# Performance work log

Hardware: AMD Instinct MI355X
Metric: run time of the kernel (lower is better)

The kernel has to match this reference:

```python
import jax, jax.numpy as jnp
import numpy as np

# Dimensions
BATCH = 4
NUM_NODE = 20000
NUM_EDGE = 1280000   # avg degree 64
K = 2                # num_rd_kernels
NUM_SEQ = 13         # num_sequence (13 time points -> 12 intervals)
SEQ_IN = 12
RES = 2              # fixed-step Euler substeps per interval (resolution)
TEMP = 1.0           # temperature for gate softmax
NUM_OUT = -12        # num_output_sequence slice


def setup_inputs() -> dict:
    key = jax.random.key(0)
    ks = jax.random.split(key, 6)
    inputs = jax.random.normal(ks[0], (BATCH, 1, NUM_NODE, SEQ_IN), dtype=jnp.float32)
    gate = jax.random.normal(ks[1], (NUM_SEQ - 1, K), dtype=jnp.float32)
    # edge list from adjacency CSV (from/to columns)
    src = jax.random.randint(ks[2], (NUM_EDGE,), 0, NUM_NODE)
    dst = jax.random.randint(ks[3], (NUM_EDGE,), 0, NUM_NODE)
    # learned per-kernel parameters of multi_reaction_diffusion
    w = jax.random.normal(ks[4], (K, NUM_EDGE), dtype=jnp.float32) * 0.1  # edge diffusivity logits
    r = jax.random.normal(ks[5], (K, NUM_NODE), dtype=jnp.float32) * 0.1  # node reaction coeffs
    return {"inputs": inputs, "gate": gate, "w": w, "r": r, "src": src, "dst": dst}


def _dxdt(x, g, w, r, src, dst):
    # x: [B,N]  g: [K]  w: [K,E]  r: [K,N]
    a = jax.nn.sigmoid(w)                                   # [K,E] edge diffusivity
    xs = x[:, src]                                          # [B,E]
    xd = x[:, dst]                                          # [B,E]
    msg = a[:, None, :] * (xs - xd)[None, :, :]             # [K,B,E]
    # scatter-add messages into destination nodes
    diff = jax.ops.segment_sum(jnp.moveaxis(msg, 2, 0), dst, num_segments=NUM_NODE)  # [N,K,B]
    diff = jnp.transpose(diff, (1, 2, 0))                   # [K,B,N]
    react = r[:, None, :] * x[None] * (1.0 - x[None])       # [K,B,N] logistic reaction
    return jnp.einsum('k,kbn->bn', g, diff + react)         # gate-weighted mix of RD kernels


def reference(inputs, gate, w, r, src, dst):
    x0 = inputs[:, 0, :, -1]                                # [B,N]
    dt = 1.0 / (NUM_SEQ - 1)
    h = jnp.float32(dt / RES)
    gates = jax.nn.softmax(gate / TEMP, axis=-1)            # [NUM_SEQ-1, K]

    def interval(x, g):
        def step(xc, _):
            return xc + h * _dxdt(xc, g, w, r, src, dst), None
        x, _ = jax.lax.scan(step, x, None, length=RES)
        return x, x

    _, traj = jax.lax.scan(interval, x0, gates)             # [NUM_SEQ-1, B, N]
    out = jnp.concatenate([x0[None], traj], axis=0)         # [NUM_SEQ, B, N]
    return out[NUM_OUT:]                                    # last 12 horizons
```

## Files before the change

kernel.cpp:

```cpp
#include <hip/hip_runtime.h>
#include <hip/hip_fp16.h>
#include <math.h>

#define NNODE 20000
#define NEDGE 1280000
#define HSTEP (1.0f/24.0f)
#define NBUCK 313
#define CAP   4608
#define EPB   2048

__global__ void rd_init(const float* __restrict__ inp,
                        float4* __restrict__ x,
                        int* __restrict__ cursor) {
    int n = blockIdx.x * blockDim.x + threadIdx.x;
    if (n < NBUCK) cursor[n] = n * CAP;
    if (n < NNODE) {
        float4 v;
        v.x = inp[0 * NNODE * 12 + n * 12 + 11];
        v.y = inp[1 * NNODE * 12 + n * 12 + 11];
        v.z = inp[2 * NNODE * 12 + n * 12 + 11];
        v.w = inp[3 * NNODE * 12 + n * 12 + 11];
        x[n] = v;
    }
}

__global__ __launch_bounds__(256) void rd_part(const int* __restrict__ src,
                                               const int* __restrict__ dst,
                                               const float* __restrict__ w,
                                               int* __restrict__ cursor,
                                               uint2* __restrict__ rec) {
    __shared__ int h[4][NBUCK];
    int wv = threadIdx.x >> 6;
    for (int i = threadIdx.x; i < 4 * NBUCK; i += 256) ((int*)h)[i] = 0;
    __syncthreads();
    int e0 = blockIdx.x * EPB;
    #pragma unroll
    for (int k = 0; k < 8; ++k) {
        int e = e0 + k * 256 + threadIdx.x;
        if (e < NEDGE) atomicAdd(&h[wv][dst[e] >> 6], 1);
    }
    __syncthreads();
    for (int i = threadIdx.x; i < NBUCK; i += 256) {
        int c0 = h[0][i], c1 = h[1][i], c2 = h[2][i], c3 = h[3][i];
        int tot = c0 + c1 + c2 + c3;
        int gb = tot ? atomicAdd(&cursor[i], tot) : 0;
        h[0][i] = gb;
        h[1][i] = gb + c0;
        h[2][i] = gb + c0 + c1;
        h[3][i] = gb + c0 + c1 + c2;
    }
    __syncthreads();
    #pragma unroll
    for (int k = 0; k < 8; ++k) {
        int e = e0 + k * 256 + threadIdx.x;
        if (e < NEDGE) {
            int d = dst[e];
            int b = d >> 6;
            int p = atomicAdd(&h[wv][b], 1);
            float s0 = 1.0f / (1.0f + expf(-w[e]));
            float s1 = 1.0f / (1.0f + expf(-w[NEDGE + e]));
            __half2 hh = __floats2half2_rn(s0, s1);
            uint2 q;
            q.x = (unsigned)src[e] | ((unsigned)(d & 63) << 16);
            q.y = *(unsigned*)&hh;
            if (p < (b + 1) * CAP) rec[p] = q;
        }
    }
}

__global__ void rd_bscan(const int* __restrict__ cursor, int* __restrict__ boff) {
    int lane = threadIdx.x;
    int carry = 0;
    #pragma unroll
    for (int c = 0; c < 5; ++c) {
        int i = c * 64 + lane;
        int v = (i < NBUCK) ? (cursor[i] - i * CAP) : 0;
        int incl = v;
        #pragma unroll
        for (int o = 1; o < 64; o <<= 1) {
            int u = __shfl_up(incl, o, 64);
            if (lane >= o) incl += u;
        }
        if (i < NBUCK) boff[i] = carry + incl - v;
        carry += __shfl(incl, 63, 64);
    }
    if (lane == 0) boff[NBUCK] = carry;
}

__global__ __launch_bounds__(256) void rd_bsort(const uint2* __restrict__ rec,
                                                const int* __restrict__ cursor,
                                                const int* __restrict__ boff,
                                                unsigned short* __restrict__ es16,
                                                unsigned* __restrict__ ew32,
                                                int* __restrict__ offsets) {
    __shared__ uint2 rs[CAP];
    __shared__ int h[64], excl[64];
    int b = blockIdx.x;
    int ib = b * CAP;
    int cnt = cursor[b] - ib; if (cnt > CAP) cnt = CAP;
    int ob = boff[b];
    if (threadIdx.x < 64) h[threadIdx.x] = 0;
    __syncthreads();
    for (int i = threadIdx.x; i < cnt; i += 256) {
        uint2 q = rec[ib + i];
        rs[i] = q;
        atomicAdd(&h[(q.x >> 16) & 63], 1);
    }
    __syncthreads();
    if (threadIdx.x < 64) {
        int lane = threadIdx.x;
        int v = h[lane];
        int incl = v;
        #pragma unroll
        for (int o = 1; o < 64; o <<= 1) {
            int u = __shfl_up(incl, o, 64);
            if (lane >= o) incl += u;
        }
        excl[lane] = incl - v;
        int n = b * 64 + lane;
        if (n < NNODE) offsets[n] = ob + excl[lane];
        h[lane] = 0;
    }
    if (b == NBUCK - 1 && threadIdx.x == 0) offsets[NNODE] = NEDGE;
    __syncthreads();
    for (int i = threadIdx.x; i < cnt; i += 256) {
        uint2 q = rs[i];
        int dl = (q.x >> 16) & 63;
        int rank = atomicAdd(&h[dl], 1);
        int p = ob + excl[dl] + rank;
        es16[p] = (unsigned short)(q.x & 0xFFFFu);
        ew32[p] = q.y;
    }
}

__global__ __launch_bounds__(256) void rd_step(
        const float4* __restrict__ xin, float4* __restrict__ xout,
        const unsigned short* __restrict__ es16,
        const unsigned* __restrict__ ew32,
        const int* __restrict__ offsets,
        const float* __restrict__ r, const float* __restrict__ gate,
        int itv, int write_out, float* __restrict__ out) {
    int tid  = blockIdx.x * 256 + threadIdx.x;
    int node = tid >> 4;
    int sub  = threadIdx.x & 15;
    float ga = gate[2 * itv], gb = gate[2 * itv + 1];
    float g0 = 1.0f / (1.0f + expf(gb - ga));
    float g1 = 1.0f - g0;

    int beg = offsets[node], end = offsets[node + 1];
    float4 acc = make_float4(0.f, 0.f, 0.f, 0.f);
    float wsum = 0.f;

    int j = beg + sub;
    bool valid = j < end;
    unsigned s = 0, wb = 0;
    if (valid) { s = es16[j]; wb = ew32[j]; }
    while (valid) {
        float4 xs = xin[s];
        int jn = j + 16;
        bool vn = jn < end;
        unsigned s2 = 0, wb2 = 0;
        if (vn) { s2 = es16[jn]; wb2 = ew32[jn]; }
        __half2 hh = *(__half2*)&wb;
        float2 f = __half22float2(hh);
        float we = fmaf(g0, f.x, g1 * f.y);
        acc.x = fmaf(we, xs.x, acc.x);
        acc.y = fmaf(we, xs.y, acc.y);
        acc.z = fmaf(we, xs.z, acc.z);
        acc.w = fmaf(we, xs.w, acc.w);
        wsum += we;
        j = jn; s = s2; wb = wb2; valid = vn;
    }
    #pragma unroll
    for (int m = 8; m >= 1; m >>= 1) {
        acc.x += __shfl_xor(acc.x, m, 64);
        acc.y += __shfl_xor(acc.y, m, 64);
        acc.z += __shfl_xor(acc.z, m, 64);
        acc.w += __shfl_xor(acc.w, m, 64);
        wsum  += __shfl_xor(wsum,  m, 64);
    }
    float4 xd = xin[node];
    float rc = fmaf(g0, r[node], g1 * r[NNODE + node]);
    float4 xn;
    xn.x = xd.x + HSTEP * ((acc.x - wsum * xd.x) + rc * xd.x * (1.0f - xd.x));
    xn.y = xd.y + HSTEP * ((acc.y - wsum * xd.y) + rc * xd.y * (1.0f - xd.y));
    xn.z = xd.z + HSTEP * ((acc.z - wsum * xd.z) + rc * xd.z * (1.0f - xd.z));
    xn.w = xd.w + HSTEP * ((acc.w - wsum * xd.w) + rc * xd.w * (1.0f - xd.w));
    if (sub == 0) xout[node] = xn;
    if (write_out && sub < 4) {
        float v = (sub == 0) ? xn.x : (sub == 1) ? xn.y : (sub == 2) ? xn.z : xn.w;
        out[(itv * 4 + sub) * NNODE + node] = v;
    }
}

extern "C" void kernel_launch(void* const* d_in, const int* in_sizes, int n_in,
                              void* d_out, int out_size, void* d_ws, size_t ws_size,
                              hipStream_t stream) {
    const float* inp  = (const float*)d_in[0];
    const float* gate = (const float*)d_in[1];
    const float* w    = (const float*)d_in[2];
    const float* r    = (const float*)d_in[3];
    const int*   src  = (const int*)d_in[4];
    const int*   dst  = (const int*)d_in[5];
    float* out = (float*)d_out;

    char* ws = (char*)d_ws;
    float4*         xA      = (float4*)(ws + 0);
    float4*         xB      = (float4*)(ws + 320512);
    int*            offsets = (int*)   (ws + 641024);
    int*            cursor  = (int*)   (ws + 721152);
    int*            boff    = (int*)   (ws + 722432);
    uint2*          rec     = (uint2*) (ws + 723712);
    unsigned short* es16    = (unsigned short*)(ws + 12262144);
    unsigned*       ew32    = (unsigned*)(ws + 14822144);

    rd_init <<<(NNODE + 255) / 256, 256, 0, stream>>>(inp, xA, cursor);
    rd_part <<<(NEDGE + EPB - 1) / EPB, 256, 0, stream>>>(src, dst, w, cursor, rec);
    rd_bscan<<<1, 64, 0, stream>>>(cursor, boff);
    rd_bsort<<<NBUCK, 256, 0, stream>>>(rec, cursor, boff, es16, ew32, offsets);

    float4* xin = xA;
    float4* xout = xB;
    for (int itv = 0; itv < 12; ++itv) {
        for (int s = 0; s < 2; ++s) {
            rd_step<<<NNODE * 16 / 256, 256, 0, stream>>>(xin, xout, es16, ew32,
                                                          offsets, r, gate, itv, s, out);
            float4* t = xin; xin = xout; xout = t;
        }
    }
}
```

Baseline: 265.2 us.

## Vectorize edge partitioning, cache ranks in LDS, widen bsort, unroll gather loop

```diff
diff --git a/kernel.cpp b/kernel.cpp
--- a/kernel.cpp
+++ b/kernel.cpp
@@ -24,23 +24,32 @@
     }
 }
 
-__global__ __launch_bounds__(256) void rd_part(const int* __restrict__ src,
-                                               const int* __restrict__ dst,
-                                               const float* __restrict__ w,
+__global__ __launch_bounds__(256) void rd_part(const int4* __restrict__ src4,
+                                               const int4* __restrict__ dst4,
+                                               const float4* __restrict__ w4,
                                                int* __restrict__ cursor,
                                                uint2* __restrict__ rec) {
     __shared__ int h[4][NBUCK];
-    int wv = threadIdx.x >> 6;
-    for (int i = threadIdx.x; i < 4 * NBUCK; i += 256) ((int*)h)[i] = 0;
-    __syncthreads();
-    int e0 = blockIdx.x * EPB;
-    #pragma unroll
-    for (int k = 0; k < 8; ++k) {
-        int e = e0 + k * 256 + threadIdx.x;
-        if (e < NEDGE) atomicAdd(&h[wv][dst[e] >> 6], 1);
-    }
-    __syncthreads();
-    for (int i = threadIdx.x; i < NBUCK; i += 256) {
+    __shared__ uint4 cache[EPB / 4];
+    int t = threadIdx.x, wv = t >> 6;
+    for (int i = t; i < 4 * NBUCK; i += 256) ((int*)h)[i] = 0;
+    __syncthreads();
+    int q0 = blockIdx.x * (EPB / 4);
+    #pragma unroll
+    for (int k = 0; k < 2; ++k) {
+        int qi = q0 + k * 256 + t;
+        int4 d4 = dst4[qi];
+        int dd[4] = {d4.x, d4.y, d4.z, d4.w};
+        unsigned cc[4];
+        #pragma unroll
+        for (int u = 0; u < 4; ++u) {
+            int rank = atomicAdd(&h[wv][dd[u] >> 6], 1);
+            cc[u] = (unsigned)dd[u] | ((unsigned)rank << 15);
+        }
+        cache[k * 256 + t] = make_uint4(cc[0], cc[1], cc[2], cc[3]);
+    }
+    __syncthreads();
+    for (int i = t; i < NBUCK; i += 256) {
         int c0 = h[0][i], c1 = h[1][i], c2 = h[2][i], c3 = h[3][i];
         int tot = c0 + c1 + c2 + c3;
         int gb = tot ? atomicAdd(&cursor[i], tot) : 0;
@@ -51,19 +60,29 @@
     }
     __syncthreads();
     #pragma unroll
-    for (int k = 0; k < 8; ++k) {
-        int e = e0 + k * 256 + threadIdx.x;
-        if (e < NEDGE) {
-            int d = dst[e];
+    for (int k = 0; k < 2; ++k) {
+        int qi = q0 + k * 256 + t;
+        int4 s4 = src4[qi];
+        float4 wa = w4[qi];
+        float4 wb = w4[NEDGE / 4 + qi];
+        uint4 c4 = cache[k * 256 + t];
+        int ss[4] = {s4.x, s4.y, s4.z, s4.w};
+        float fa[4] = {wa.x, wa.y, wa.z, wa.w};
+        float fb[4] = {wb.x, wb.y, wb.z, wb.w};
+        unsigned cc[4] = {c4.x, c4.y, c4.z, c4.w};
+        #pragma unroll
+        for (int u = 0; u < 4; ++u) {
+            int d = cc[u] & 0x7FFF;
+            int rank = (int)(cc[u] >> 15);
             int b = d >> 6;
-            int p = atomicAdd(&h[wv][b], 1);
-            float s0 = 1.0f / (1.0f + expf(-w[e]));
-            float s1 = 1.0f / (1.0f + expf(-w[NEDGE + e]));
+            int p = h[wv][b] + rank;
+            float s0 = 1.0f / (1.0f + expf(-fa[u]));
+            float s1 = 1.0f / (1.0f + expf(-fb[u]));
             __half2 hh = __floats2half2_rn(s0, s1);
-            uint2 q;
-            q.x = (unsigned)src[e] | ((unsigned)(d & 63) << 16);
-            q.y = *(unsigned*)&hh;
-            if (p < (b + 1) * CAP) rec[p] = q;
+            uint2 rq;
+            rq.x = (unsigned)ss[u] | ((unsigned)(d & 63) << 16);
+            rq.y = *(unsigned*)&hh;
+            if (p < (b + 1) * CAP) rec[p] = rq;
         }
     }
 }
@@ -87,7 +106,7 @@
     if (lane == 0) boff[NBUCK] = carry;
 }
 
-__global__ __launch_bounds__(256) void rd_bsort(const uint2* __restrict__ rec,
+__global__ __launch_bounds__(512) void rd_bsort(const uint2* __restrict__ rec,
                                                 const int* __restrict__ cursor,
                                                 const int* __restrict__ boff,
                                                 unsigned short* __restrict__ es16,
@@ -101,7 +120,7 @@
     int ob = boff[b];
     if (threadIdx.x < 64) h[threadIdx.x] = 0;
     __syncthreads();
-    for (int i = threadIdx.x; i < cnt; i += 256) {
+    for (int i = threadIdx.x; i < cnt; i += 512) {
         uint2 q = rec[ib + i];
         rs[i] = q;
         atomicAdd(&h[(q.x >> 16) & 63], 1);
@@ -123,7 +142,7 @@
     }
     if (b == NBUCK - 1 && threadIdx.x == 0) offsets[NNODE] = NEDGE;
     __syncthreads();
-    for (int i = threadIdx.x; i < cnt; i += 256) {
+    for (int i = threadIdx.x; i < cnt; i += 512) {
         uint2 q = rs[i];
         int dl = (q.x >> 16) & 63;
         int rank = atomicAdd(&h[dl], 1);
@@ -148,28 +167,55 @@
     float g1 = 1.0f - g0;
 
     int beg = offsets[node], end = offsets[node + 1];
+    float4 xd = xin[node];
+    float rc = fmaf(g0, r[node], g1 * r[NNODE + node]);
+
     float4 acc = make_float4(0.f, 0.f, 0.f, 0.f);
     float wsum = 0.f;
-
     int j = beg + sub;
-    bool valid = j < end;
-    unsigned s = 0, wb = 0;
-    if (valid) { s = es16[j]; wb = ew32[j]; }
-    while (valid) {
-        float4 xs = xin[s];
-        int jn = j + 16;
-        bool vn = jn < end;
-        unsigned s2 = 0, wb2 = 0;
-        if (vn) { s2 = es16[jn]; wb2 = ew32[jn]; }
-        __half2 hh = *(__half2*)&wb;
-        float2 f = __half22float2(hh);
-        float we = fmaf(g0, f.x, g1 * f.y);
-        acc.x = fmaf(we, xs.x, acc.x);
-        acc.y = fmaf(we, xs.y, acc.y);
-        acc.z = fmaf(we, xs.z, acc.z);
-        acc.w = fmaf(we, xs.w, acc.w);
-        wsum += we;
-        j = jn; s = s2; wb = wb2; valid = vn;
+    for (; j + 48 < end; j += 64) {
+        unsigned a0 = es16[j], a1 = es16[j + 16], a2 = es16[j + 32], a3 = es16[j + 48];
+        unsigned b0 = ew32[j], b1 = ew32[j + 16], b2 = ew32[j + 32], b3 = ew32[j + 48];
+        float4 x0 = xin[a0], x1 = xin[a1], x2 = xin[a2], x3 = xin[a3];
+        float2 f0 = __half22float2(*(__half2*)&b0);
+        float2 f1 = __half22float2(*(__half2*)&b1);
+        float2 f2 = __half22float2(*(__half2*)&b2);
+        float2 f3 = __half22float2(*(__half2*)&b3);
+        float we0 = fmaf(g0, f0.x, g1 * f0.y);
+        float we1 = fmaf(g0, f1.x, g1 * f1.y);
+        float we2 = fmaf(g0, f2.x, g1 * f2.y);
+        float we3 = fmaf(g0, f3.x, g1 * f3.y);
+        acc.x = fmaf(we0, x0.x, fmaf(we1, x1.x, fmaf(we2, x2.x, fmaf(we3, x3.x, acc.x))));
+        acc.y = fmaf(we0, x0.y, fmaf(we1, x1.y, fmaf(we2, x2.y, fmaf(we3, x3.y, acc.y))));
+        acc.z = fmaf(we0, x0.z, fmaf(we1, x1.z, fmaf(we2, x2.z, fmaf(we3, x3.z, acc.z))));
+        acc.w = fmaf(we0, x0.w, fmaf(we1, x1.w, fmaf(we2, x2.w, fmaf(we3, x3.w, acc.w))));
+        wsum += (we0 + we1) + (we2 + we3);
+    }
+    for (; j + 16 < end; j += 32) {
+        unsigned a0 = es16[j], a1 = es16[j + 16];
+        unsigned b0 = ew32[j], b1 = ew32[j + 16];
+        float4 x0 = xin[a0], x1 = xin[a1];
+        float2 f0 = __half22float2(*(__half2*)&b0);
+        float2 f1 = __half22float2(*(__half2*)&b1);
+        float we0 = fmaf(g0, f0.x, g1 * f0.y);
+        float we1 = fmaf(g0, f1.x, g1 * f1.y);
+        acc.x = fmaf(we0, x0.x, fmaf(we1, x1.x, acc.x));
+        acc.y = fmaf(we0, x0.y, fmaf(we1, x1.y, acc.y));
+        acc.z = fmaf(we0, x0.z, fmaf(we1, x1.z, acc.z));
+        acc.w = fmaf(we0, x0.w, fmaf(we1, x1.w, acc.w));
+        wsum += we0 + we1;
+    }
+    if (j < end) {
+        unsigned a0 = es16[j];
+        unsigned b0 = ew32[j];
+        float4 x0 = xin[a0];
+        float2 f0 = __half22float2(*(__half2*)&b0);
+        float we0 = fmaf(g0, f0.x, g1 * f0.y);
+        acc.x = fmaf(we0, x0.x, acc.x);
+        acc.y = fmaf(we0, x0.y, acc.y);
+        acc.z = fmaf(we0, x0.z, acc.z);
+        acc.w = fmaf(we0, x0.w, acc.w);
+        wsum += we0;
     }
     #pragma unroll
     for (int m = 8; m >= 1; m >>= 1) {
@@ -179,8 +225,6 @@
         acc.w += __shfl_xor(acc.w, m, 64);
         wsum  += __shfl_xor(wsum,  m, 64);
     }
-    float4 xd = xin[node];
-    float rc = fmaf(g0, r[node], g1 * r[NNODE + node]);
     float4 xn;
     xn.x = xd.x + HSTEP * ((acc.x - wsum * xd.x) + rc * xd.x * (1.0f - xd.x));
     xn.y = xd.y + HSTEP * ((acc.y - wsum * xd.y) + rc * xd.y * (1.0f - xd.y));
@@ -215,9 +259,10 @@
     unsigned*       ew32    = (unsigned*)(ws + 14822144);
 
     rd_init <<<(NNODE + 255) / 256, 256, 0, stream>>>(inp, xA, cursor);
-    rd_part <<<(NEDGE + EPB - 1) / EPB, 256, 0, stream>>>(src, dst, w, cursor, rec);
+    rd_part <<<NEDGE / EPB, 256, 0, stream>>>((const int4*)src, (const int4*)dst,
+                                              (const float4*)w, cursor, rec);
     rd_bscan<<<1, 64, 0, stream>>>(cursor, boff);
-    rd_bsort<<<NBUCK, 256, 0, stream>>>(rec, cursor, boff, es16, ew32, offsets);
+    rd_bsort<<<NBUCK, 512, 0, stream>>>(rec, cursor, boff, es16, ew32, offsets);
 
     float4* xin = xA;
     float4* xout = xB;
```

Result: faster. 252.4 us (-4.8%).
